# Kernel optimization log

Measured on AMD Instinct MI355X. Metric: run time of the kernel, lower is better.

The kernel has to match this reference:

```python
import jax, jax.numpy as jnp
import numpy as np

N_NODES = 30000
N_REL = 8
N_EDGES = 131072
IN_FEAT = 512
OUT_FEAT = 512


def setup_inputs() -> dict:
    key = jax.random.key(0)
    k1, k2, k3, k4, k5 = jax.random.split(key, 5)
    x = jax.random.normal(k1, (N_NODES, IN_FEAT), dtype=jnp.float32)
    # per-relation weights [R, in, out] (xavier-ish scale)
    weight = jax.random.normal(k2, (N_REL, IN_FEAT, OUT_FEAT), dtype=jnp.float32) * (2.0 / (IN_FEAT + OUT_FEAT)) ** 0.5
    loop_weight = jax.random.normal(k3, (IN_FEAT, OUT_FEAT), dtype=jnp.float32) * (2.0 / (IN_FEAT + OUT_FEAT)) ** 0.5
    h_bias = jnp.zeros((OUT_FEAT,), dtype=jnp.float32)
    src = jax.random.randint(k4, (N_REL, N_EDGES), 0, N_NODES, dtype=jnp.int32)
    dst = jax.random.randint(k5, (N_REL, N_EDGES), 0, N_NODES, dtype=jnp.int32)
    return {"x": x, "weight": weight, "loop_weight": loop_weight,
            "h_bias": h_bias, "src": src, "dst": dst}


def reference(x, weight, loop_weight, h_bias, src, dst):
    # Per-relation GraphConv(norm='right', weight=W_r):
    #   transform all node feats, gather on src, scatter-sum on dst,
    #   normalize by in-degree (clamped to 1). Relations summed (HeteroGraphConv 'sum').
    xw = jnp.einsum('ni,rio->rno', x, weight)  # [R, N, out]

    def per_rel(xw_r, src_r, dst_r):
        msgs = xw_r[src_r]  # [E, out] gathered messages
        agg = jax.ops.segment_sum(msgs, dst_r, num_segments=N_NODES)
        deg = jax.ops.segment_sum(jnp.ones_like(dst_r, dtype=xw_r.dtype), dst_r,
                                  num_segments=N_NODES)
        return agg / jnp.clip(deg, 1.0)[:, None]

    h = jax.vmap(per_rel)(xw, src, dst).sum(axis=0)  # [N, out]
    h = h + x @ loop_weight + h_bias  # self-loop + bias
    return jax.nn.relu(h)  # activation; dropout=0.0 -> identity
```

## Files before the change

### kernel.cpp

```cpp
#include <hip/hip_runtime.h>
#include <hip/hip_bf16.h>

#define N_NODES 30000
#define N_REL   8
#define N_EDGES 131072
#define FEAT    512
#define KTOT    4608
#define CAP     32

typedef __attribute__((ext_vector_type(8))) __bf16 v8bf;
typedef __attribute__((ext_vector_type(4))) __bf16 v4bf;
typedef __attribute__((ext_vector_type(4))) float  v4f;
typedef __attribute__((ext_vector_type(2))) float  f2;
typedef __attribute__((ext_vector_type(8))) unsigned short u16x8;

static __device__ __forceinline__ void load_lds16(const void* g, void* l) {
  __builtin_amdgcn_global_load_lds(
      (const __attribute__((address_space(1))) void*)g,
      (__attribute__((address_space(3))) void*)l, 16, 0, 0);
}

#define CONV_BLOCKS 15000
#define TR_BLOCKS   2304
#define CNT_BLOCKS  512
__global__ __launch_bounds__(256)
void k_prep(const float* __restrict__ x, const float* __restrict__ w,
            const float* __restrict__ lw, const int* __restrict__ src,
            const int* __restrict__ dst, __bf16* __restrict__ xbf,
            __bf16* __restrict__ Wt, int* __restrict__ cnt,
            unsigned short* __restrict__ slots) {
  __shared__ float t[32][33];
  const int b = blockIdx.x, tid = threadIdx.x;
  if (b < CONV_BLOCKS) {
    int i = b * 256 + tid;
    float4 v = ((const float4*)x)[i];
    v4bf o;
    o[0] = (__bf16)v.x; o[1] = (__bf16)v.y; o[2] = (__bf16)v.z; o[3] = (__bf16)v.w;
    ((v4bf*)xbf)[i] = o;
  } else if (b < CONV_BLOCKS + TR_BLOCKS) {
    int tb = b - CONV_BLOCKS;
    int k0 = (tb % 144) * 32, n0 = (tb / 144) * 32;
    int tx = tid & 31, ty = tid >> 5;
    #pragma unroll
    for (int q = 0; q < 4; ++q) {
      int k = k0 + ty + q * 8, n = n0 + tx;
      float v = (k < 4096) ? w[(size_t)k * 512 + n] : lw[(size_t)(k - 4096) * 512 + n];
      t[ty + q * 8][tx] = v;
    }
    __syncthreads();
    #pragma unroll
    for (int q = 0; q < 4; ++q) {
      int n = n0 + ty + q * 8, k = k0 + tx;
      Wt[(size_t)n * KTOT + k] = (__bf16)t[tx][ty + q * 8];
    }
  } else {
    int cb  = b - CONV_BLOCKS - TR_BLOCKS;
    int rel = cb & 7;
    int q   = cb >> 3;
    int e0  = rel * N_EDGES + (q * 256 + tid) * 8;
    int4 sa = *(const int4*)(src + e0), sb = *(const int4*)(src + e0 + 4);
    int4 da = *(const int4*)(dst + e0), db = *(const int4*)(dst + e0 + 4);
    int ss[8] = {sa.x, sa.y, sa.z, sa.w, sb.x, sb.y, sb.z, sb.w};
    int dd[8] = {da.x, da.y, da.z, da.w, db.x, db.y, db.z, db.w};
    int bb[8], pp[8];
    #pragma unroll
    for (int j = 0; j < 8; ++j) {
      bb[j] = rel * N_NODES + dd[j];
      pp[j] = atomicAdd(&cnt[bb[j]], 1);
    }
    #pragma unroll
    for (int j = 0; j < 8; ++j)
      if (pp[j] < CAP) slots[(size_t)bb[j] * CAP + pp[j]] = (unsigned short)ss[j];
  }
}

__global__ __launch_bounds__(256)
void k_agg_slice(const __bf16* __restrict__ xbf, const int* __restrict__ cnt,
                 const unsigned short* __restrict__ slots,
                 __bf16* __restrict__ out, int nBuckets, int bps) {
  const int bid   = blockIdx.x;
  const int slice = bid / bps;
  const int ib    = bid - slice * bps;
  const int tid   = threadIdx.x;
  const int wave  = tid >> 6, lane = tid & 63;
  const int grp   = lane >> 3;
  const int li    = lane & 7;
  const int w     = ib * 32 + wave * 8 + grp;
  const bool valid = (w < nBuckets);

  int c = 0;
  u16x8 qs[4];
  if (valid) {
    c = cnt[w];
    const unsigned short* sl = slots + (size_t)w * CAP;
    qs[0] = *(const u16x8*)(sl);
    qs[1] = *(const u16x8*)(sl + 8);
    qs[2] = *(const u16x8*)(sl + 16);
    qs[3] = *(const u16x8*)(sl + 24);
  }
  int cc = c < CAP ? c : CAP;
  int cmax = cc;
  cmax = max(cmax, __shfl_xor(cmax, 8));
  cmax = max(cmax, __shfl_xor(cmax, 16));
  cmax = max(cmax, __shfl_xor(cmax, 32));

  const __bf16* xb = xbf + slice * 64 + (size_t)li * 8;
  f2 acc2[4];
  #pragma unroll
  for (int p = 0; p < 4; ++p) acc2[p] = (f2){0.f, 0.f};
  #pragma unroll
  for (int g = 0; g < 4; ++g) {
    if (cmax > g * 8) {
      v8bf r[8];
      #pragma unroll
      for (int j = 0; j < 8; ++j)
        if (cc > g * 8 + j)
          r[j] = *(const v8bf*)(xb + (size_t)qs[g][j] * FEAT);
      #pragma unroll
      for (int j = 0; j < 8; ++j)
        if (cc > g * 8 + j) {
          const unsigned* ru = (const unsigned*)&r[j];
          #pragma unroll
          for (int p = 0; p < 4; ++p) {
            f2 v;
            v[0] = __uint_as_float(ru[p] << 16);
            v[1] = __uint_as_float(ru[p] & 0xffff0000u);
            acc2[p] += v;
          }
        }
    }
  }
  if (valid) {
    float scale = 1.0f / (float)(c > 1 ? c : 1);
    v8bf o;
    #pragma unroll
    for (int p = 0; p < 4; ++p) {
      o[2 * p]     = (__bf16)(acc2[p][0] * scale);
      o[2 * p + 1] = (__bf16)(acc2[p][1] * scale);
    }
    *(v8bf*)(out + (size_t)w * FEAT + slice * 64 + (size_t)li * 8) = o;
  }
}

__global__ __launch_bounds__(256)
void k_aggregate(const __bf16* __restrict__ xbf, const int* __restrict__ cnt,
                 const unsigned short* __restrict__ slots,
                 __bf16* __restrict__ out, int nBuckets) {
  int w = (blockIdx.x * blockDim.x + threadIdx.x) >> 6;
  int lane = threadIdx.x & 63;
  if (w >= nBuckets) return;
  const unsigned short* sl = slots + (size_t)w * CAP;
  u16x8 qs[4];
  qs[0] = *(const u16x8*)(sl);
  qs[1] = *(const u16x8*)(sl + 8);
  qs[2] = *(const u16x8*)(sl + 16);
  qs[3] = *(const u16x8*)(sl + 24);
  int c = cnt[w];
  int cc = c < CAP ? c : CAP;
  const __bf16* xb = xbf + (size_t)lane * 8;
  f2 acc2[4];
  #pragma unroll
  for (int p = 0; p < 4; ++p) acc2[p] = (f2){0.f, 0.f};
  #pragma unroll
  for (int g = 0; g < 4; ++g) {
    if (cc > g * 8) {
      int m = cc - g * 8;
      v8bf r[8];
      #pragma unroll
      for (int j = 0; j < 8; ++j)
        if (m > j) r[j] = *(const v8bf*)(xb + (size_t)qs[g][j] * FEAT);
      #pragma unroll
      for (int j = 0; j < 8; ++j)
        if (m > j) {
          const unsigned* ru = (const unsigned*)&r[j];
          #pragma unroll
          for (int p = 0; p < 4; ++p) {
            f2 v;
            v[0] = __uint_as_float(ru[p] << 16);
            v[1] = __uint_as_float(ru[p] & 0xffff0000u);
            acc2[p] += v;
          }
        }
    }
  }
  float scale = 1.0f / (float)(c > 1 ? c : 1);
  v8bf o;
  #pragma unroll
  for (int p = 0; p < 4; ++p) {
    o[2 * p]     = (__bf16)(acc2[p][0] * scale);
    o[2 * p + 1] = (__bf16)(acc2[p][1] * scale);
  }
  *(v8bf*)(out + (size_t)w * FEAT + lane * 8) = o;
}

#define A_SLOT_E 16384
#define B_BASE_E 49152

template <bool ACCUM, bool FINAL>
__global__ __launch_bounds__(512, 2)
void k_gemm3(const __bf16* __restrict__ A, size_t slabStride,
             const __bf16* __restrict__ Wt, int kTiles,
             const float* __restrict__ bias, float* __restrict__ C) {
  __shared__ __align__(16) char smem[163840];
  __bf16* lds = (__bf16*)smem;

  const int tid  = threadIdx.x;
  const int wave = tid >> 6, lane = tid & 63;
  const int lr = lane >> 3, lc = lane & 7;
  const int gcs = (lc ^ lr) * 8;
  const int quad = lane >> 4, l15 = lane & 15;
  const int wR2 = wave >> 2;
  const int wC4 = wave & 3;

  const int nwg = gridDim.x;
  const int qq = nwg >> 3, rr = nwg & 7;
  const int xcd = blockIdx.x & 7, oidx = blockIdx.x >> 3;
  const int wg = (xcd < rr ? xcd * (qq + 1) : rr * (qq + 1) + (xcd - rr) * qq) + oidx;
  const int mtile = wg >> 1, ntile = wg & 1;
  const int mBase = mtile * 256, nBase = ntile * 256;

  v4f acc[2][2][4][2];
  #pragma unroll
  for (int a = 0; a < 2; ++a)
    #pragma unroll
    for (int bq = 0; bq < 2; ++bq)
      #pragma unroll
      for (int mi = 0; mi < 4; ++mi)
        #pragma unroll
        for (int ni = 0; ni < 2; ++ni)
          acc[a][bq][mi][ni] = (v4f){0.f, 0.f, 0.f, 0.f};

  auto stageA = [&](int t, int h) {
    __bf16* dst = lds + (t % 3) * A_SLOT_E;
    const int kk = t * 64;
    const __bf16* base = A + (size_t)(kk >> 9) * slabStride + (kk & 511);
    #pragma unroll
    for (int r2 = 0; r2 < 2; ++r2) {
      int rt = h * 128 + r2 * 64 + wave * 8;
      int row = mBase + rt + lr;
      if (row > N_NODES - 1) row = N_NODES - 1;
      load_lds16(base + (size_t)row * FEAT + gcs, dst + rt * 64);
    }
  };
  auto stageB = [&](int t, int h) {
    __bf16* dst = lds + B_BASE_E + (t & 1) * A_SLOT_E;
    const int kk = t * 64;
    #pragma unroll
    for (int r2 = 0; r2 < 2; ++r2) {
      int rt = h * 128 + r2 * 64 + wave * 8;
      int n = nBase + rt + lr;
      load_lds16(Wt + (size_t)n * KTOT + kk + gcs, dst + rt * 64);
    }
  };

  stageA(0, 0); stageA(0, 1);
  stageB(0, 0); stageB(0, 1);
  if (kTiles > 1) {
    stageA(1, 0); stageA(1, 1);
    asm volatile("s_waitcnt vmcnt(4)" ::: "memory");
  } else {
    asm volatile("s_waitcnt vmcnt(0)" ::: "memory");
  }
  __builtin_amdgcn_s_barrier();
  __builtin_amdgcn_sched_barrier(0);

  for (int t = 0; t < kTiles; ++t) {
    const __bf16* sA = lds + (t % 3) * A_SLOT_E;
    const __bf16* sB = lds + B_BASE_E + (t & 1) * A_SLOT_E;
    const bool pfB = (t + 1) < kTiles;
    const bool pfA = (t + 2) < kTiles;
    v8bf af[4][2], bf0[2][2], bf1[2][2];

    #pragma unroll
    for (int mi = 0; mi < 4; ++mi)
      #pragma unroll
      for (int ks = 0; ks < 2; ++ks) {
        int m = wR2 * 64 + mi * 16 + l15;
        int q = ks * 4 + quad;
        af[mi][ks] = *(const v8bf*)(sA + m * 64 + ((q ^ (m & 7)) * 8));
      }
    #pragma unroll
    for (int ni = 0; ni < 2; ++ni)
      #pragma unroll
      for (int ks = 0; ks < 2; ++ks) {
        int n = wC4 * 32 + ni * 16 + l15;
        int q = ks * 4 + quad;
        bf0[ni][ks] = *(const v8bf*)(sB + n * 64 + ((q ^ (n & 7)) * 8));
      }
    if (pfB) stageB(t + 1, 0);
    __builtin_amdgcn_s_barrier();
    asm volatile("s_waitcnt lgkmcnt(0)" ::: "memory");
    __builtin_amdgcn_sched_barrier(0);
    __builtin_amdgcn_s_setprio(1);
    #pragma unroll
    for (int ks = 0; ks < 2; ++ks)
      #pragma unroll
      for (int mi = 0; mi < 4; ++mi)
        #pragma unroll
        for (int ni = 0; ni < 2; ++ni)
          acc[0][0][mi][ni] = __builtin_amdgcn_mfma_f32_16x16x32_bf16(
              af[mi][ks], bf0[ni][ks], acc[0][0][mi][ni], 0, 0, 0);
    __builtin_amdgcn_s_setprio(0);
    if (pfB) asm volatile("s_waitcnt vmcnt(6)" ::: "memory");
    else     asm volatile("s_waitcnt vmcnt(0)" ::: "memory");
    __builtin_amdgcn_s_barrier();
    __builtin_amdgcn_sched_barrier(0);

    #pragma unroll
    for (int ni = 0; ni < 2; ++ni)
      #pragma unroll
      for (int ks = 0; ks < 2; ++ks) {
        int n = 128 + wC4 * 32 + ni * 16 + l15;
        int q = ks * 4 + quad;
        bf1[ni][ks] = *(const v8bf*)(sB + n * 64 + ((q ^ (n & 7)) * 8));
      }
    if (pfB) stageB(t + 1, 1);
    __builtin_amdgcn_s_barrier();
    asm volatile("s_waitcnt lgkmcnt(0)" ::: "memory");
    __builtin_amdgcn_sched_barrier(0);
    __builtin_amdgcn_s_setprio(1);
    #pragma unroll
    for (int ks = 0; ks < 2; ++ks)
      #pragma unroll
      for (int mi = 0; mi < 4; ++mi)
        #pragma unroll
        for (int ni = 0; ni < 2; ++ni)
          acc[0][1][mi][ni] = __builtin_amdgcn_mfma_f32_16x16x32_bf16(
              af[mi][ks], bf1[ni][ks], acc[0][1][mi][ni], 0, 0, 0);
    __builtin_amdgcn_s_setprio(0);
    __builtin_amdgcn_s_barrier();
    __builtin_amdgcn_sched_barrier(0);

    #pragma unroll
    for (int mi = 0; mi < 4; ++mi)
      #pragma unroll
      for (int ks = 0; ks < 2; ++ks) {
        int m = 128 + wR2 * 64 + mi * 16 + l15;
        int q = ks * 4 + quad;
        af[mi][ks] = *(const v8bf*)(sA + m * 64 + ((q ^ (m & 7)) * 8));
      }
    if (pfA) stageA(t + 2, 0);
    __builtin_amdgcn_s_barrier();
    asm volatile("s_waitcnt lgkmcnt(0)" ::: "memory");
    __builtin_amdgcn_sched_barrier(0);
    __builtin_amdgcn_s_setprio(1);
    #pragma unroll
    for (int ks = 0; ks < 2; ++ks)
      #pragma unroll
      for (int mi = 0; mi < 4; ++mi)
        #pragma unroll
        for (int ni = 0; ni < 2; ++ni)
          acc[1][1][mi][ni] = __builtin_amdgcn_mfma_f32_16x16x32_bf16(
              af[mi][ks], bf1[ni][ks], acc[1][1][mi][ni], 0, 0, 0);
    __builtin_amdgcn_s_setprio(0);
    __builtin_amdgcn_s_barrier();
    __builtin_amdgcn_sched_barrier(0);

    if (pfA) stageA(t + 2, 1);
    __builtin_amdgcn_s_barrier();
    __builtin_amdgcn_s_setprio(1);
    #pragma unroll
    for (int ks = 0; ks < 2; ++ks)
      #pragma unroll
      for (int mi = 0; mi < 4; ++mi)
        #pragma unroll
        for (int ni = 0; ni < 2; ++ni)
          acc[1][0][mi][ni] = __builtin_amdgcn_mfma_f32_16x16x32_bf16(
              af[mi][ks], bf0[ni][ks], acc[1][0][mi][ni], 0, 0, 0);
    __builtin_amdgcn_s_setprio(0);
    if (pfA)      asm volatile("s_waitcnt vmcnt(6)" ::: "memory");
    else if (pfB) asm volatile("s_waitcnt vmcnt(2)" ::: "memory");
    __builtin_amdgcn_s_barrier();
    __builtin_amdgcn_sched_barrier(0);
  }

  asm volatile("s_waitcnt vmcnt(0)" ::: "memory");
  float* cbuf = (float*)smem;
  const int f4 = tid & 63;
  const int colg = nBase + f4 * 4;
  v4f bias4 = (v4f){0.f, 0.f, 0.f, 0.f};
  if (FINAL) bias4 = *(const v4f*)(bias + colg);
  #pragma unroll
  for (int h = 0; h < 4; ++h) {
    __syncthreads();
    if (wR2 == (h & 1)) {
      const int R = h >> 1;
      #pragma unroll
      for (int Cq = 0; Cq < 2; ++Cq)
        #pragma unroll
        for (int mi = 0; mi < 4; ++mi)
          #pragma unroll
          for (int ni = 0; ni < 2; ++ni)
            #pragma unroll
            for (int e = 0; e < 4; ++e)
              cbuf[(mi * 16 + quad * 4 + e) * 260 + Cq * 128 + wC4 * 32 + ni * 16 + l15] =
                  acc[R][Cq][mi][ni][e];
    }
    __syncthreads();
    #pragma unroll
    for (int i = 0; i < 8; ++i) {
      int rl  = i * 8 + (tid >> 6);
      int row = mBase + h * 64 + rl;
      if (row < N_NODES) {
        v4f v = *(const v4f*)(cbuf + rl * 260 + f4 * 4);
        size_t idx = (size_t)row * FEAT + colg;
        if (ACCUM) v += *(const v4f*)(C + idx);
        if (FINAL) {
          #pragma unroll
          for (int e = 0; e < 4; ++e) v[e] = fmaxf(v[e] + bias4[e], 0.f);
        }
        *(v4f*)(C + idx) = v;
      }
    }
  }
}

template <bool ACCUM, bool FINAL>
__global__ __launch_bounds__(256, 4)
void k_gemm(const __bf16* __restrict__ A, size_t slabStride,
            const __bf16* __restrict__ Wt, int wtStride, int kTiles,
            const float* __restrict__ bias, float* __restrict__ C,
            int mtBase, int mtEnd) {
  __shared__ __align__(16) char smem[33792];
  __bf16* As = (__bf16*)smem;
  __bf16* Bs = (__bf16*)(smem + 16384);

  const int tid  = threadIdx.x;
  const int wave = tid >> 6;
  const int lane = tid & 63;
  const int lr = lane >> 3, lc = lane & 7;
  const int gcs = (lc ^ lr) * 8;
  const int quad = lane >> 4, l15 = lane & 15;
  const int wRow = wave >> 1, wCol = wave & 1;

  const int panel = blockIdx.x >> 5;
  const int w32   = blockIdx.x & 31;
  const int mtile = mtBase + panel * 8 + (w32 & 7);
  const int ntile = w32 >> 3;
  if (mtile >= mtEnd) return;
  const int mBase = mtile * 128;
  const int nBase = ntile * 128;

  v4f acc[4][4];
  #pragma unroll
  for (int i = 0; i < 4; ++i)
    #pragma unroll
    for (int j = 0; j < 4; ++j) acc[i][j] = (v4f){0.f, 0.f, 0.f, 0.f};

  for (int kt = 0; kt < kTiles; ++kt) {
    const int kk = kt * 64;
    const __bf16* aT = A + (size_t)(kk >> 9) * slabStride + (kk & 511);
    #pragma unroll
    for (int t = 0; t < 4; ++t) {
      int chunk = wave * 4 + t;
      int row = mBase + chunk * 8 + lr;
      if (row > N_NODES - 1) row = N_NODES - 1;
      load_lds16(aT + (size_t)row * FEAT + gcs, As + chunk * 512);
      int n = nBase + chunk * 8 + lr;
      load_lds16(Wt + (size_t)n * wtStride + kk + gcs, Bs + chunk * 512);
    }
    __syncthreads();
    #pragma unroll
    for (int ks = 0; ks < 2; ++ks) {
      const int q = ks * 4 + quad;
      v8bf af[4], bfr[4];
      #pragma unroll
      for (int mi = 0; mi < 4; ++mi) {
        int m = wRow * 64 + mi * 16 + l15;
        af[mi] = *(const v8bf*)(As + m * 64 + ((q ^ (m & 7)) * 8));
      }
      #pragma unroll
      for (int ni = 0; ni < 4; ++ni) {
        int n = wCol * 64 + ni * 16 + l15;
        bfr[ni] = *(const v8bf*)(Bs + n * 64 + ((q ^ (n & 7)) * 8));
      }
      #pragma unroll
      for (int mi = 0; mi < 4; ++mi)
        #pragma unroll
        for (int ni = 0; ni < 4; ++ni)
          acc[mi][ni] = __builtin_amdgcn_mfma_f32_16x16x32_bf16(af[mi], bfr[ni], acc[mi][ni], 0, 0, 0);
    }
    __syncthreads();
  }

  float* cbuf = (float*)smem;
  const int f4c  = tid & 31;
  const int colg = nBase + f4c * 4;
  v4f bias4 = (v4f){0.f, 0.f, 0.f, 0.f};
  if (FINAL) bias4 = *(const v4f*)(bias + colg);
  #pragma unroll
  for (int h = 0; h < 2; ++h) {
    if (wRow == h) {
      #pragma unroll
      for (int mi = 0; mi < 4; ++mi) {
        int r0 = mi * 16 + quad * 4;
        #pragma unroll
        for (int ni = 0; ni < 4; ++ni) {
          int c = wCol * 64 + ni * 16 + l15;
          #pragma unroll
          for (int e = 0; e < 4; ++e)
            cbuf[(r0 + e) * 132 + c] = acc[mi][ni][e];
        }
      }
    }
    __syncthreads();
    #pragma unroll
    for (int i = 0; i < 8; ++i) {
      int rh  = (tid >> 5) + 8 * i;
      int row = mBase + h * 64 + rh;
      if (row < N_NODES) {
        v4f v = *(const v4f*)(cbuf + rh * 132 + f4c * 4);
        size_t idx = (size_t)row * FEAT + colg;
        if (ACCUM) v += *(const v4f*)(C + idx);
        if (FINAL) {
          #pragma unroll
          for (int e = 0; e < 4; ++e) v[e] = fmaxf(v[e] + bias4[e], 0.f);
        }
        *(v4f*)(C + idx) = v;
      }
    }
    __syncthreads();
  }
}

extern "C" void kernel_launch(void* const* d_in, const int* in_sizes, int n_in,
                              void* d_out, int out_size, void* d_ws, size_t ws_size,
                              hipStream_t stream) {
  const float* x    = (const float*)d_in[0];
  const float* w    = (const float*)d_in[1];
  const float* lw   = (const float*)d_in[2];
  const float* bias = (const float*)d_in[3];
  const int*   src  = (const int*)d_in[4];
  const int*   dst  = (const int*)d_in[5];
  float* out = (float*)d_out;

  char* ws = (char*)d_ws;
  const size_t SLAB  = (size_t)N_NODES * FEAT;
  const size_t slabB = SLAB * 2;
  const size_t wtB   = (size_t)FEAT * KTOT * 2;
  const size_t cntB  = (size_t)N_REL * N_NODES * 4;
  const size_t slotB = (size_t)N_REL * N_NODES * CAP * 2;
  const size_t fixedB = wtB + cntB + slotB;

  __bf16*         Wt     = (__bf16*)ws;
  int*            cnt    = (int*)(ws + wtB);
  unsigned short* slots  = (unsigned short*)(ws + wtB + cntB);
  __bf16*         slabs  = (__bf16*)(ws + fixedB);

  int nSlab = (int)((ws_size - fixedB) / slabB);
  int g = nSlab - 1;
  if (g > 7) g = 7;
  if (g < 1) g = 1;
  __bf16* xbf = slabs + (size_t)g * SLAB;

  hipMemsetAsync(cnt, 0, cntB, stream);
  k_prep<<<CONV_BLOCKS + TR_BLOCKS + CNT_BLOCKS, 256, 0, stream>>>(
      x, w, lw, src, dst, xbf, Wt, cnt, slots);

  if (g == 7) {
    const int mt256 = (N_NODES + 255) / 256;
    const int grid3 = mt256 * 2;
    const int bps1 = (7 * N_NODES + 31) / 32;
    k_agg_slice<<<8 * bps1, 256, 0, stream>>>(xbf, cnt, slots,
                                              slabs, 7 * N_NODES, bps1);
    k_gemm3<false, false><<<grid3, 512, 0, stream>>>(
        slabs, SLAB, Wt, 3584 / 64, bias, out);
    const int bps2 = (N_NODES + 31) / 32;
    k_agg_slice<<<8 * bps2, 256, 0, stream>>>(
        xbf, cnt + 7 * N_NODES, slots + (size_t)7 * N_NODES * CAP,
        slabs + (size_t)6 * SLAB, N_NODES, bps2);
    k_gemm3<true, true><<<grid3, 512, 0, stream>>>(
        slabs + (size_t)6 * SLAB, SLAB, Wt + 3584, 1024 / 64, bias, out);
  } else {
    const int nMtiles = (N_NODES + 127) / 128;
    const int gemmGrid = ((nMtiles + 7) / 8) * 32;
    for (int r0 = 0; r0 < N_REL; r0 += g) {
      int gc2 = (N_REL - r0) < g ? (N_REL - r0) : g;
      k_aggregate<<<(gc2 * N_NODES) / 4, 256, 0, stream>>>(
          xbf, cnt + r0 * N_NODES, slots + (size_t)r0 * N_NODES * CAP,
          slabs, gc2 * N_NODES);
      if (r0 == 0)
        k_gemm<false, false><<<gemmGrid, 256, 0, stream>>>(
            slabs, SLAB, Wt + r0 * 512, KTOT, gc2 * 8, bias, out, 0, nMtiles);
      else
        k_gemm<true, false><<<gemmGrid, 256, 0, stream>>>(
            slabs, SLAB, Wt + r0 * 512, KTOT, gc2 * 8, bias, out, 0, nMtiles);
    }
    k_gemm<true, true><<<gemmGrid, 256, 0, stream>>>(xbf, SLAB, Wt + 4096, KTOT,
                                                     8, bias, out, 0, nMtiles);
  }
}
```

Measured before the change: 498.2 us.

## Simplify GEMM main loop to two compute phases with one barrier per tile

Replaces the hand-scheduled four-quadrant MFMA loop with a two-phase loop. Each phase loads one A half plus both B halves and issues the MFMAs for two accumulator quadrants. The loop now has a single barrier per k-tile instead of many, and the B prefetch moves to the start of the iteration. Scheduling barriers, priority hints and explicit lgkmcnt waits are removed and instruction ordering is left to the compiler. This cuts synchronisation overhead, but raises register pressure because more fragments stay live at once, and it may lose the carefully interleaved overlap of loads and MFMAs.

```diff
diff --git a/kernel.cpp b/kernel.cpp
--- a/kernel.cpp
+++ b/kernel.cpp
@@ -252,6 +252,16 @@
       load_lds16(Wt + (size_t)n * KTOT + kk + gcs, dst + rt * 64);
     }
   };
+  auto rdA = [&](const __bf16* sA, int half, int mi, int ks) -> v8bf {
+    int m = half * 128 + wR2 * 64 + mi * 16 + l15;
+    int q = ks * 4 + quad;
+    return *(const v8bf*)(sA + m * 64 + ((q ^ (m & 7)) * 8));
+  };
+  auto rdB = [&](const __bf16* sB, int half, int ni, int ks) -> v8bf {
+    int n = half * 128 + wC4 * 32 + ni * 16 + l15;
+    int q = ks * 4 + quad;
+    return *(const v8bf*)(sB + n * 64 + ((q ^ (n & 7)) * 8));
+  };
 
   stageA(0, 0); stageA(0, 1);
   stageB(0, 0); stageB(0, 1);
@@ -262,119 +272,62 @@
     asm volatile("s_waitcnt vmcnt(0)" ::: "memory");
   }
   __builtin_amdgcn_s_barrier();
-  __builtin_amdgcn_sched_barrier(0);
 
   for (int t = 0; t < kTiles; ++t) {
     const __bf16* sA = lds + (t % 3) * A_SLOT_E;
     const __bf16* sB = lds + B_BASE_E + (t & 1) * A_SLOT_E;
     const bool pfB = (t + 1) < kTiles;
     const bool pfA = (t + 2) < kTiles;
-    v8bf af[4][2], bf0[2][2], bf1[2][2];
-
+
+    if (pfB) { stageB(t + 1, 0); stageB(t + 1, 1); }
+
+    v8bf a0[4][2], a1[4][2], b0[2][2], b1[2][2];
     #pragma unroll
     for (int mi = 0; mi < 4; ++mi)
       #pragma unroll
+      for (int ks = 0; ks < 2; ++ks) a0[mi][ks] = rdA(sA, 0, mi, ks);
+    #pragma unroll
+    for (int ni = 0; ni < 2; ++ni)
+      #pragma unroll
       for (int ks = 0; ks < 2; ++ks) {
-        int m = wR2 * 64 + mi * 16 + l15;
-        int q = ks * 4 + quad;
-        af[mi][ks] = *(const v8bf*)(sA + m * 64 + ((q ^ (m & 7)) * 8));
+        b0[ni][ks] = rdB(sB, 0, ni, ks);
+        b1[ni][ks] = rdB(sB, 1, ni, ks);
       }
-    #pragma unroll
-    for (int ni = 0; ni < 2; ++ni)
-      #pragma unroll
-      for (int ks = 0; ks < 2; ++ks) {
-        int n = wC4 * 32 + ni * 16 + l15;
-        int q = ks * 4 + quad;
-        bf0[ni][ks] = *(const v8bf*)(sB + n * 64 + ((q ^ (n & 7)) * 8));
-      }
-    if (pfB) stageB(t + 1, 0);
-    __builtin_amdgcn_s_barrier();
-    asm volatile("s_waitcnt lgkmcnt(0)" ::: "memory");
-    __builtin_amdgcn_sched_barrier(0);
-    __builtin_amdgcn_s_setprio(1);
     #pragma unroll
     for (int ks = 0; ks < 2; ++ks)
       #pragma unroll
       for (int mi = 0; mi < 4; ++mi)
         #pragma unroll
-        for (int ni = 0; ni < 2; ++ni)
+        for (int ni = 0; ni < 2; ++ni) {
           acc[0][0][mi][ni] = __builtin_amdgcn_mfma_f32_16x16x32_bf16(
-              af[mi][ks], bf0[ni][ks], acc[0][0][mi][ni], 0, 0, 0);
-    __builtin_amdgcn_s_setprio(0);
-    if (pfB) asm volatile("s_waitcnt vmcnt(6)" ::: "memory");
+              a0[mi][ks], b0[ni][ks], acc[0][0][mi][ni], 0, 0, 0);
+          acc[0][1][mi][ni] = __builtin_amdgcn_mfma_f32_16x16x32_bf16(
+              a0[mi][ks], b1[ni][ks], acc[0][1][mi][ni], 0, 0, 0);
+        }
+
+    if (pfA) { stageA(t + 2, 0); stageA(t + 2, 1); }
+
+    #pragma unroll
+    for (int mi = 0; mi < 4; ++mi)
+      #pragma unroll
+      for (int ks = 0; ks < 2; ++ks) a1[mi][ks] = rdA(sA, 1, mi, ks);
+    #pragma unroll
+    for (int ks = 0; ks < 2; ++ks)
+      #pragma unroll
+      for (int mi = 0; mi < 4; ++mi)
+        #pragma unroll
+        for (int ni = 0; ni < 2; ++ni) {
+          acc[1][1][mi][ni] = __builtin_amdgcn_mfma_f32_16x16x32_bf16(
+              a1[mi][ks], b1[ni][ks], acc[1][1][mi][ni], 0, 0, 0);
+          acc[1][0][mi][ni] = __builtin_amdgcn_mfma_f32_16x16x32_bf16(
+              a1[mi][ks], b0[ni][ks], acc[1][0][mi][ni], 0, 0, 0);
+        }
+
+    if (pfA) asm volatile("s_waitcnt vmcnt(4)" ::: "memory");
     else     asm volatile("s_waitcnt vmcnt(0)" ::: "memory");
     __builtin_amdgcn_s_barrier();
-    __builtin_amdgcn_sched_barrier(0);
-
-    #pragma unroll
-    for (int ni = 0; ni < 2; ++ni)
-      #pragma unroll
-      for (int ks = 0; ks < 2; ++ks) {
-        int n = 128 + wC4 * 32 + ni * 16 + l15;
-        int q = ks * 4 + quad;
-        bf1[ni][ks] = *(const v8bf*)(sB + n * 64 + ((q ^ (n & 7)) * 8));
-      }
-    if (pfB) stageB(t + 1, 1);
-    __builtin_amdgcn_s_barrier();
-    asm volatile("s_waitcnt lgkmcnt(0)" ::: "memory");
-    __builtin_amdgcn_sched_barrier(0);
-    __builtin_amdgcn_s_setprio(1);
-    #pragma unroll
-    for (int ks = 0; ks < 2; ++ks)
-      #pragma unroll
-      for (int mi = 0; mi < 4; ++mi)
-        #pragma unroll
-        for (int ni = 0; ni < 2; ++ni)
-          acc[0][1][mi][ni] = __builtin_amdgcn_mfma_f32_16x16x32_bf16(
-              af[mi][ks], bf1[ni][ks], acc[0][1][mi][ni], 0, 0, 0);
-    __builtin_amdgcn_s_setprio(0);
-    __builtin_amdgcn_s_barrier();
-    __builtin_amdgcn_sched_barrier(0);
-
-    #pragma unroll
-    for (int mi = 0; mi < 4; ++mi)
-      #pragma unroll
-      for (int ks = 0; ks < 2; ++ks) {
-        int m = 128 + wR2 * 64 + mi * 16 + l15;
-        int q = ks * 4 + quad;
-        af[mi][ks] = *(const v8bf*)(sA + m * 64 + ((q ^ (m & 7)) * 8));
-      }
-    if (pfA) stageA(t + 2, 0);
-    __builtin_amdgcn_s_barrier();
-    asm volatile("s_waitcnt lgkmcnt(0)" ::: "memory");
-    __builtin_amdgcn_sched_barrier(0);
-    __builtin_amdgcn_s_setprio(1);
-    #pragma unroll
-    for (int ks = 0; ks < 2; ++ks)
-      #pragma unroll
-      for (int mi = 0; mi < 4; ++mi)
-        #pragma unroll
-        for (int ni = 0; ni < 2; ++ni)
-          acc[1][1][mi][ni] = __builtin_amdgcn_mfma_f32_16x16x32_bf16(
-              af[mi][ks], bf1[ni][ks], acc[1][1][mi][ni], 0, 0, 0);
-    __builtin_amdgcn_s_setprio(0);
-    __builtin_amdgcn_s_barrier();
-    __builtin_amdgcn_sched_barrier(0);
-
-    if (pfA) stageA(t + 2, 1);
-    __builtin_amdgcn_s_barrier();
-    __builtin_amdgcn_s_setprio(1);
-    #pragma unroll
-    for (int ks = 0; ks < 2; ++ks)
-      #pragma unroll
-      for (int mi = 0; mi < 4; ++mi)
-        #pragma unroll
-        for (int ni = 0; ni < 2; ++ni)
-          acc[1][0][mi][ni] = __builtin_amdgcn_mfma_f32_16x16x32_bf16(
-              af[mi][ks], bf0[ni][ks], acc[1][0][mi][ni], 0, 0, 0);
-    __builtin_amdgcn_s_setprio(0);
-    if (pfA)      asm volatile("s_waitcnt vmcnt(6)" ::: "memory");
-    else if (pfB) asm volatile("s_waitcnt vmcnt(2)" ::: "memory");
-    __builtin_amdgcn_s_barrier();
-    __builtin_amdgcn_sched_barrier(0);
-  }
-
-  asm volatile("s_waitcnt vmcnt(0)" ::: "memory");
+  }
+
   float* cbuf = (float*)smem;
   const int f4 = tid & 63;
   const int colg = nBase + f4 * 4;
```

Result: faster. 479.1 us (-3.8%).
